# Performance work log

Measured on AMD Instinct MI355X. Metric: run time of the kernel, lower is better.

## Reference

```python
import jax, jax.numpy as jnp
import numpy as np

TEMPERATURE = 0.1
B, D, A = 8192, 256, 4


def setup_inputs() -> dict:
    key = jax.random.key(0)
    k1, k2 = jax.random.split(key)
    # scale by 1/sqrt(D) so dot products are O(1) and exp(sim/T) is finite
    embeddings = jax.random.normal(k1, (B, D), dtype=jnp.float32) / jnp.sqrt(jnp.float32(D))
    labels = jax.random.randint(k2, (B, A), 0, 6, dtype=jnp.int64)
    return {"embeddings": embeddings, "labels": labels}


def reference(embeddings, labels):
    b = embeddings.shape[0]
    # [B, B] similarity scaled by temperature
    sim = jnp.matmul(embeddings, embeddings.T) / TEMPERATURE
    # positive mask: ANY aspect matches (vectorized over aspects), diagonal zeroed
    pos_mask = jnp.any(labels[:, None, :] == labels[None, :, :], axis=-1)
    pos_mask = pos_mask & ~jnp.eye(b, dtype=bool)
    pos_mask = pos_mask.astype(sim.dtype)

    exp_sim = jnp.exp(sim)
    positive_sim = jnp.sum(exp_sim * pos_mask, axis=1)            # [B]
    all_sim = jnp.sum(exp_sim, axis=1) - jnp.diagonal(exp_sim)   # [B]

    valid = positive_sim > 0
    pos_safe = jnp.where(valid, positive_sim, 1.0)
    all_safe = jnp.where(valid, all_sim, 1.0)
    row_loss = jnp.where(valid, -jnp.log(pos_safe / (all_safe + 1e-8)), 0.0)

    num_pos = jnp.sum(valid.astype(sim.dtype))
    loss = jnp.where(num_pos > 0, jnp.sum(row_loss) / jnp.maximum(num_pos, 1.0), 0.0)
    return loss
```

## Files before the change

kernel.cpp:

```cpp
#include <hip/hip_runtime.h>
#include <stdint.h>

typedef short short8 __attribute__((ext_vector_type(8)));
typedef float f32x4 __attribute__((ext_vector_type(4)));
typedef float f32x2 __attribute__((ext_vector_type(2)));

#define B_TOTAL 8192
#define DDIM 256
#define BM 256
#define BN 64
#define NSPLIT 16
#define COLS_PER (B_TOTAL / NSPLIT)
#define ITERS (COLS_PER / BN)
#define NBLOCKS ((B_TOTAL / BM) * NSPLIT)
#define SCALE_HALF 3.79828546f
#define LN2F 0.6931471805599453f

typedef __attribute__((address_space(3))) char lds_char;
typedef __attribute__((address_space(1))) const char gbl_char;

__device__ __forceinline__ unsigned short f2bf(float f) {
  unsigned int u = __builtin_bit_cast(unsigned int, f);
  u = (u + 0x7FFFu + ((u >> 16) & 1u)) >> 16;
  return (unsigned short)u;
}

__global__ __launch_bounds__(256) void prep_all(
    const float* __restrict__ E, const int* __restrict__ lab,
    unsigned short* __restrict__ Eb, unsigned int* __restrict__ plab,
    float* __restrict__ posAll) {
  const int t = blockIdx.x * 256 + threadIdx.x;
  const float4* s4 = (const float4*)E + (size_t)t * 2;
  float4 v0 = s4[0], v1 = s4[1];
  short8 o;
  o[0] = (short)f2bf(v0.x * SCALE_HALF); o[1] = (short)f2bf(v0.y * SCALE_HALF);
  o[2] = (short)f2bf(v0.z * SCALE_HALF); o[3] = (short)f2bf(v0.w * SCALE_HALF);
  o[4] = (short)f2bf(v1.x * SCALE_HALF); o[5] = (short)f2bf(v1.y * SCALE_HALF);
  o[6] = (short)f2bf(v1.z * SCALE_HALF); o[7] = (short)f2bf(v1.w * SCALE_HALF);
  *(short8*)(Eb + (size_t)t * 8) = o;
  if (t < B_TOTAL) {
    int4 l = ((const int4*)lab)[t];
    plab[t] = (1u << ((unsigned)l.x & 31u))
            | (1u << (((unsigned)l.y & 31u) + 6u))
            | (1u << (((unsigned)l.z & 31u) + 12u))
            | (1u << (((unsigned)l.w & 31u) + 18u));
  }
  if (t < 2 * B_TOTAL) posAll[t] = 0.0f;
}

struct __align__(16) SMem {
  char btile[2][BN * DDIM * 2];
  unsigned int plab_all[COLS_PER];
};

template <int DIAG>
__device__ __forceinline__ void do_epilogue(
    const f32x4 (&acc)[4][2], int colbase, int it, int l15,
    const unsigned int (&pi)[2][4], const int (&irow)[2][4],
    const unsigned int* plab_all, f32x2 (&pos2)[2][2], f32x2 (&all2)[2][2]) {
#pragma unroll
  for (int n = 0; n < 4; ++n) {
    const int j = colbase + n * 16 + l15;
    const unsigned int hj = plab_all[it * BN + n * 16 + l15];
#pragma unroll
    for (int m = 0; m < 2; ++m) {
      float e[4];
#pragma unroll
      for (int q = 0; q < 4; ++q) {
        float v = __builtin_amdgcn_exp2f(acc[n][m][q]);
        if (DIAG) { if (j == irow[m][q]) v = 0.0f; }
        e[q] = v;
      }
      f32x2 p01 = { (pi[m][0] & hj) ? e[0] : 0.0f, (pi[m][1] & hj) ? e[1] : 0.0f };
      f32x2 p23 = { (pi[m][2] & hj) ? e[2] : 0.0f, (pi[m][3] & hj) ? e[3] : 0.0f };
      all2[m][0] += (f32x2){e[0], e[1]};
      all2[m][1] += (f32x2){e[2], e[3]};
      pos2[m][0] += p01;
      pos2[m][1] += p23;
    }
  }
}

__global__ __launch_bounds__(512, 2) void main_kernel(
    const unsigned short* __restrict__ Eb, const unsigned int* __restrict__ plab,
    float* __restrict__ posArr, float* __restrict__ allArr) {
  __shared__ SMem sm;
  const int tid = threadIdx.x;
  const int lane = tid & 63;
  const int wid = tid >> 6;
  const int l15 = lane & 15;
  const int l4 = lane >> 4;
  const int rb = (int)blockIdx.x & 31;
  const int cs = (int)blockIdx.x >> 5;
  const int rowbase = rb * BM;
  const int colstart = cs * COLS_PER;

  auto stage = [&](int bufi, int cb) {
#pragma unroll
    for (int q = 0; q < 4; ++q) {
      const unsigned int base = (unsigned int)q * 8192u + (unsigned int)wid * 1024u;
      const unsigned int L = base + (unsigned int)lane * 16u;
      const unsigned int r = L >> 9;
      const unsigned int s = (L >> 4) & 31u;
      const unsigned int c = s ^ (r & 7u);
      const char* src = (const char*)(Eb + (size_t)(cb + (int)r) * DDIM + c * 8);
      char* dst = sm.btile[bufi] + base;
      __builtin_amdgcn_global_load_lds((gbl_char*)src, (lds_char*)dst, 16, 0, 0);
    }
  };

  stage(0, colstart);

  short8 afrag[2][8];
#pragma unroll
  for (int m = 0; m < 2; ++m) {
    const int row = rowbase + wid * 32 + m * 16 + l15;
    const unsigned short* rp = Eb + (size_t)row * DDIM + l4 * 8;
#pragma unroll
    for (int k = 0; k < 8; ++k) afrag[m][k] = *(const short8*)(rp + k * 32);
  }

  sm.plab_all[tid] = plab[colstart + tid];

  unsigned int pi[2][4];
  int irow[2][4];
#pragma unroll
  for (int m = 0; m < 2; ++m)
#pragma unroll
    for (int q = 0; q < 4; ++q) {
      const int i = rowbase + wid * 32 + m * 16 + l4 * 4 + q;
      irow[m][q] = i;
      pi[m][q] = plab[i];
    }

  asm volatile("s_waitcnt lgkmcnt(0)" ::: "memory");
  __builtin_amdgcn_sched_barrier(0);

  f32x2 pos2[2][2] = {};
  f32x2 all2[2][2] = {};

  for (int it = 0; it < ITERS; ++it) {
    const int colbase = colstart + it * BN;
    const int cur = it & 1;

    if (it + 1 < ITERS) {
      stage(cur ^ 1, colbase + BN);
      asm volatile("s_waitcnt vmcnt(4)" ::: "memory");
    } else {
      asm volatile("s_waitcnt vmcnt(0)" ::: "memory");
    }
    __builtin_amdgcn_s_barrier();
    __builtin_amdgcn_sched_barrier(0);

    f32x4 acc[4][2];
#pragma unroll
    for (int n = 0; n < 4; ++n)
#pragma unroll
      for (int m = 0; m < 2; ++m) acc[n][m] = (f32x4){0.f, 0.f, 0.f, 0.f};

    __builtin_amdgcn_s_setprio(1);
#pragma unroll
    for (int k = 0; k < 8; ++k) {
      short8 b[4];
#pragma unroll
      for (int n = 0; n < 4; ++n) {
        const unsigned int rr = (unsigned int)(n * 16 + l15);
        const unsigned int cdx = (unsigned int)(k * 4 + l4);
        const unsigned int s = cdx ^ (rr & 7u);
        b[n] = *(const short8*)(sm.btile[cur] + rr * 512u + s * 16u);
      }
#pragma unroll
      for (int n = 0; n < 4; ++n)
#pragma unroll
        for (int m = 0; m < 2; ++m)
          acc[n][m] = __builtin_amdgcn_mfma_f32_16x16x32_bf16(
              afrag[m][k], b[n], acc[n][m], 0, 0, 0);
    }
    __builtin_amdgcn_s_setprio(0);

    const bool hasDiag = (colbase < rowbase + BM) && (rowbase < colbase + BN);
    if (hasDiag)
      do_epilogue<1>(acc, colbase, it, l15, pi, irow, sm.plab_all, pos2, all2);
    else
      do_epilogue<0>(acc, colbase, it, l15, pi, irow, sm.plab_all, pos2, all2);

    __builtin_amdgcn_s_barrier();
    __builtin_amdgcn_sched_barrier(0);
  }

#pragma unroll
  for (int m = 0; m < 2; ++m)
#pragma unroll
    for (int q = 0; q < 4; ++q) {
      float p = pos2[m][q >> 1][q & 1], al = all2[m][q >> 1][q & 1];
      p += __shfl_xor(p, 1); p += __shfl_xor(p, 2);
      p += __shfl_xor(p, 4); p += __shfl_xor(p, 8);
      al += __shfl_xor(al, 1); al += __shfl_xor(al, 2);
      al += __shfl_xor(al, 4); al += __shfl_xor(al, 8);
      if (l15 == 0) {
        atomicAdd(&posArr[irow[m][q]], p);
        atomicAdd(&allArr[irow[m][q]], al);
      }
    }
}

__global__ __launch_bounds__(1024) void finalize_kernel(
    const float* __restrict__ posArr, const float* __restrict__ allArr,
    float* __restrict__ out) {
  float ls = 0.f, cnt = 0.f;
#pragma unroll
  for (int k = 0; k < B_TOTAL / 1024; ++k) {
    const int i = threadIdx.x + (k << 10);
    const float p = posArr[i];
    const float a = allArr[i];
    if (p > 0.f) {
      ls += (__builtin_amdgcn_logf(a + 1e-8f) - __builtin_amdgcn_logf(p)) * LN2F;
      cnt += 1.f;
    }
  }
#pragma unroll
  for (int msk = 1; msk < 64; msk <<= 1) {
    ls += __shfl_xor(ls, msk);
    cnt += __shfl_xor(cnt, msk);
  }
  __shared__ float sls[16], scnt[16];
  const int w = threadIdx.x >> 6;
  if ((threadIdx.x & 63) == 0) { sls[w] = ls; scnt[w] = cnt; }
  __syncthreads();
  if (threadIdx.x == 0) {
    float L = 0.f, C = 0.f;
    for (int i = 0; i < 16; ++i) { L += sls[i]; C += scnt[i]; }
    out[0] = (C > 0.f) ? L / fmaxf(C, 1.f) : 0.f;
  }
}

extern "C" void kernel_launch(void* const* d_in, const int* in_sizes, int n_in,
                              void* d_out, int out_size, void* d_ws, size_t ws_size,
                              hipStream_t stream) {
  const float* E = (const float*)d_in[0];
  const int* lab = (const int*)d_in[1];
  float* out = (float*)d_out;
  char* ws = (char*)d_ws;

  unsigned short* Eb = (unsigned short*)ws;
  unsigned int* plab = (unsigned int*)(ws + 4u * 1024u * 1024u);
  float* posArr = (float*)(ws + 4u * 1024u * 1024u + 32u * 1024u);
  float* allArr = posArr + B_TOTAL;

  prep_all<<<1024, 256, 0, stream>>>(E, lab, Eb, plab, posArr);
  main_kernel<<<NBLOCKS, 512, 0, stream>>>(Eb, plab, posArr, allArr);
  finalize_kernel<<<1, 1024, 0, stream>>>(posArr, allArr, out);
}
```

Baseline: 112.0 us.

## Interleave per-column-block MFMA loops with exp epilogue to overlap compute

Restructures each iteration so the k-loop runs separately for each 16-column sub-block n, with two accumulator sets ping-ponging. The exp/mask epilogue for one sub-block is placed between the MFMA loops of later sub-blocks, so VALU/transcendental work can overlap with matrix-core work instead of running after all MFMAs finish. It also cuts the live accumulator registers from 8 f32x4 to 4. The cost is LDS B-fragment loads issued per sub-block rather than in one batch, and more dependence on the compiler interleaving the two instruction streams.

```diff
diff --git a/kernel.cpp b/kernel.cpp
--- a/kernel.cpp
+++ b/kernel.cpp
@@ -54,31 +54,60 @@
 };
 
 template <int DIAG>
-__device__ __forceinline__ void do_epilogue(
-    const f32x4 (&acc)[4][2], int colbase, int it, int l15,
+__device__ __forceinline__ void epi_n(
+    const f32x4 (&acc)[2], int n, int colbase, int itBN, int l15,
     const unsigned int (&pi)[2][4], const int (&irow)[2][4],
-    const unsigned int* plab_all, f32x2 (&pos2)[2][2], f32x2 (&all2)[2][2]) {
-#pragma unroll
-  for (int n = 0; n < 4; ++n) {
-    const int j = colbase + n * 16 + l15;
-    const unsigned int hj = plab_all[it * BN + n * 16 + l15];
-#pragma unroll
-    for (int m = 0; m < 2; ++m) {
-      float e[4];
-#pragma unroll
-      for (int q = 0; q < 4; ++q) {
-        float v = __builtin_amdgcn_exp2f(acc[n][m][q]);
-        if (DIAG) { if (j == irow[m][q]) v = 0.0f; }
-        e[q] = v;
-      }
-      f32x2 p01 = { (pi[m][0] & hj) ? e[0] : 0.0f, (pi[m][1] & hj) ? e[1] : 0.0f };
-      f32x2 p23 = { (pi[m][2] & hj) ? e[2] : 0.0f, (pi[m][3] & hj) ? e[3] : 0.0f };
-      all2[m][0] += (f32x2){e[0], e[1]};
-      all2[m][1] += (f32x2){e[2], e[3]};
-      pos2[m][0] += p01;
-      pos2[m][1] += p23;
-    }
-  }
+    const unsigned int* __restrict__ plab_all,
+    f32x2 (&pos2)[2][2], f32x2 (&all2)[2][2]) {
+  const int j = colbase + n * 16 + l15;
+  const unsigned int hj = plab_all[itBN + n * 16 + l15];
+#pragma unroll
+  for (int m = 0; m < 2; ++m) {
+    float e[4];
+#pragma unroll
+    for (int q = 0; q < 4; ++q) {
+      float v = __builtin_amdgcn_exp2f(acc[m][q]);
+      if (DIAG) { if (j == irow[m][q]) v = 0.0f; }
+      e[q] = v;
+    }
+    f32x2 p01 = { (pi[m][0] & hj) ? e[0] : 0.0f, (pi[m][1] & hj) ? e[1] : 0.0f };
+    f32x2 p23 = { (pi[m][2] & hj) ? e[2] : 0.0f, (pi[m][3] & hj) ? e[3] : 0.0f };
+    all2[m][0] += (f32x2){e[0], e[1]};
+    all2[m][1] += (f32x2){e[2], e[3]};
+    pos2[m][0] += p01;
+    pos2[m][1] += p23;
+  }
+}
+
+template <int DIAG>
+__device__ __forceinline__ void iter_body(
+    const char* __restrict__ btile, const unsigned int* __restrict__ plab_all,
+    const short8 (&afrag)[2][8], const unsigned int (&pi)[2][4],
+    const int (&irow)[2][4], int colbase, int itBN, int l15, int l4,
+    f32x2 (&pos2)[2][2], f32x2 (&all2)[2][2]) {
+  auto kloop = [&](int n, f32x4 (&acc)[2]) {
+    acc[0] = (f32x4){0.f, 0.f, 0.f, 0.f};
+    acc[1] = (f32x4){0.f, 0.f, 0.f, 0.f};
+    const unsigned int rr = (unsigned int)(n * 16 + l15);
+#pragma unroll
+    for (int k = 0; k < 8; ++k) {
+      const unsigned int s = ((unsigned int)(k * 4 + l4)) ^ (rr & 7u);
+      short8 b = *(const short8*)(btile + rr * 512u + s * 16u);
+      acc[0] = __builtin_amdgcn_mfma_f32_16x16x32_bf16(afrag[0][k], b, acc[0], 0, 0, 0);
+      acc[1] = __builtin_amdgcn_mfma_f32_16x16x32_bf16(afrag[1][k], b, acc[1], 0, 0, 0);
+    }
+  };
+  f32x4 accA[2], accB[2];
+  __builtin_amdgcn_s_setprio(1);
+  kloop(0, accA);
+  kloop(1, accB);
+  epi_n<DIAG>(accA, 0, colbase, itBN, l15, pi, irow, plab_all, pos2, all2);
+  kloop(2, accA);
+  epi_n<DIAG>(accB, 1, colbase, itBN, l15, pi, irow, plab_all, pos2, all2);
+  kloop(3, accB);
+  __builtin_amdgcn_s_setprio(0);
+  epi_n<DIAG>(accA, 2, colbase, itBN, l15, pi, irow, plab_all, pos2, all2);
+  epi_n<DIAG>(accB, 3, colbase, itBN, l15, pi, irow, plab_all, pos2, all2);
 }
 
 __global__ __launch_bounds__(512, 2) void main_kernel(
@@ -152,37 +181,13 @@
     __builtin_amdgcn_s_barrier();
     __builtin_amdgcn_sched_barrier(0);
 
-    f32x4 acc[4][2];
-#pragma unroll
-    for (int n = 0; n < 4; ++n)
-#pragma unroll
-      for (int m = 0; m < 2; ++m) acc[n][m] = (f32x4){0.f, 0.f, 0.f, 0.f};
-
-    __builtin_amdgcn_s_setprio(1);
-#pragma unroll
-    for (int k = 0; k < 8; ++k) {
-      short8 b[4];
-#pragma unroll
-      for (int n = 0; n < 4; ++n) {
-        const unsigned int rr = (unsigned int)(n * 16 + l15);
-        const unsigned int cdx = (unsigned int)(k * 4 + l4);
-        const unsigned int s = cdx ^ (rr & 7u);
-        b[n] = *(const short8*)(sm.btile[cur] + rr * 512u + s * 16u);
-      }
-#pragma unroll
-      for (int n = 0; n < 4; ++n)
-#pragma unroll
-        for (int m = 0; m < 2; ++m)
-          acc[n][m] = __builtin_amdgcn_mfma_f32_16x16x32_bf16(
-              afrag[m][k], b[n], acc[n][m], 0, 0, 0);
-    }
-    __builtin_amdgcn_s_setprio(0);
-
     const bool hasDiag = (colbase < rowbase + BM) && (rowbase < colbase + BN);
     if (hasDiag)
-      do_epilogue<1>(acc, colbase, it, l15, pi, irow, sm.plab_all, pos2, all2);
+      iter_body<1>(sm.btile[cur], sm.plab_all, afrag, pi, irow,
+                   colbase, it * BN, l15, l4, pos2, all2);
     else
-      do_epilogue<0>(acc, colbase, it, l15, pi, irow, sm.plab_all, pos2, all2);
+      iter_body<0>(sm.btile[cur], sm.plab_all, afrag, pi, irow,
+                   colbase, it * BN, l15, l4, pos2, all2);
 
     __builtin_amdgcn_s_barrier();
     __builtin_amdgcn_sched_barrier(0);
```

After: 113.1 us. Within noise of the previous version (+1.0%).
